# Performance work log

Hardware: AMD Instinct MI355X
Metric: run time of the kernel (lower is better)

## Reference

```python
import jax, jax.numpy as jnp
import numpy as np

EPS = 1e-7  # keras.backend.epsilon()
ROUTINGS = 3


def squash(s, axis=-1):
    # standard capsule squash: ||s||^2/(1+||s||^2) * s/||s||
    n2 = jnp.sum(jnp.square(s), axis=axis, keepdims=True)
    return s * (n2 / (1.0 + n2)) / jnp.sqrt(n2 + EPS)


def setup_inputs() -> dict:
    key = jax.random.key(0)
    k1, k2 = jax.random.split(key)
    B, I, K = 32, 2048, 8          # batch, input capsules, input capsule dim
    J, D = 32, 16                  # output capsules (num_capsules), dim_capsules
    x = jax.random.normal(k1, (B, I, K), dtype=jnp.float32)
    # add_weight with random_normal_initializer(stddev=0.1), shape [J, I, D, K]
    W = 0.1 * jax.random.normal(k2, (J, I, D, K), dtype=jnp.float32)
    return {"x": x, "W": W}


def reference(x, W):
    # u_ji_hat[b,j,i,d] = sum_k W[j,i,d,k] * x[b,i,k]  (the map_fn batched matmul)
    u_hat = jnp.einsum('jidk,bik->bjid', W, x)  # [B, J, I, D]
    B, J, I, D = u_hat.shape
    b = jnp.zeros((B, J, I), dtype=u_hat.dtype)  # routing logits b_ij
    v = None
    for r in range(ROUTINGS):
        c = jax.nn.softmax(b, axis=1)                 # softmax over output capsules J
        s = jnp.einsum('bji,bjid->bjd', c, u_hat)     # weighted sum over input caps i
        v = squash(s, axis=-1)                        # squash over capsule dim (axis=-2 pre-squeeze)
        if r < ROUTINGS - 1:
            # agreement = u_hat^T v : sum over capsule dim d
            b = b + jnp.einsum('bjid,bjd->bji', u_hat, v)
    return v  # [B, J, D] == tf.squeeze(v_j, [2, 4])
```

## Files before the change

kernel.cpp:

```cpp
#include <hip/hip_runtime.h>
#include <hip/hip_fp16.h>


#define BATCH 32
#define ICAP  2048
#define KDIM  8
#define JCAP  32
#define DDIM  16
#define JD    512
#define S_ELEMS 16384
#define EPSQ  1e-7f

#define NB      256
#define ICH     8
#define ISTG    2
#define NROUND  (ICH / ISTG)
#define COLF4   66
#define SLICEF4 (16 * COLF4)

__global__ __launch_bounds__(512, 2)
void caps_pass(const float* __restrict__ W, const float* __restrict__ x,
               const float* __restrict__ vsum, __half* __restrict__ partials) {
    __shared__ float4 Wl[ISTG * SLICEF4];

    const int tid  = threadIdx.x;
    const int wave = tid >> 6;
    const int lane = tid & 63;
    const int j    = lane & 31;
    const int dh   = lane >> 5;
    const int i0   = blockIdx.x * ICH;

    float vs[4][8], sacc[4][8];
#pragma unroll
    for (int bb = 0; bb < 4; ++bb) {
        const int b = wave + 8 * bb;
        const float* vp = vsum + b * JD + j * DDIM + dh * 8;
        float4 a  = *reinterpret_cast<const float4*>(vp);
        float4 bq = *reinterpret_cast<const float4*>(vp + 4);
        vs[bb][0]=a.x; vs[bb][1]=a.y; vs[bb][2]=a.z; vs[bb][3]=a.w;
        vs[bb][4]=bq.x; vs[bb][5]=bq.y; vs[bb][6]=bq.z; vs[bb][7]=bq.w;
#pragma unroll
        for (int r = 0; r < 8; ++r) sacc[bb][r] = 0.f;
    }

    const float4* Wv = reinterpret_cast<const float4*>(W);
    int iloc_s[4], slot_s[4], gbase_s[4];
#pragma unroll
    for (int q = 0; q < 4; ++q) {
        const int f = q * 512 + tid;
        const int il = f >> 10, js = (f >> 5) & 31, c = f & 31;
        iloc_s[q]  = il;
        slot_s[q]  = il * SLICEF4 + (c & 15) * COLF4 + 2 * js + (c >> 4);
        gbase_s[q] = js * 65536 + c;
    }

    float4 pf[4];
#pragma unroll
    for (int q = 0; q < 4; ++q)
        pf[q] = Wv[gbase_s[q] + (i0 + iloc_s[q]) * 32];

    for (int rnd = 0; rnd < NROUND; ++rnd) {
        __syncthreads();
#pragma unroll
        for (int q = 0; q < 4; ++q) Wl[slot_s[q]] = pf[q];
        __syncthreads();
        if (rnd + 1 < NROUND) {
            const int gi_n = i0 + (rnd + 1) * ISTG;
#pragma unroll
            for (int q = 0; q < 4; ++q)
                pf[q] = Wv[gbase_s[q] + (gi_n + iloc_s[q]) * 32];
        }

#pragma unroll
        for (int il = 0; il < ISTG; ++il) {
            const int gi = i0 + rnd * ISTG + il;

            float4 w4[16];
            const int rbase = il * SLICEF4 + 2 * j + dh;
#pragma unroll
            for (int cp = 0; cp < 16; ++cp)
                w4[cp] = Wl[rbase + cp * COLF4];

#pragma unroll
            for (int bb = 0; bb < 4; ++bb) {
                const int b = wave + 8 * bb;
                const float* xp = x + ((size_t)b * ICAP + gi) * KDIM;
                const float4 x0 = *reinterpret_cast<const float4*>(xp);
                const float4 x1 = *reinterpret_cast<const float4*>(xp + 4);

                float u[8], tpart = 0.f;
#pragma unroll
                for (int r = 0; r < 8; ++r) {
                    const float4 wa = w4[2 * r], wb = w4[2 * r + 1];
                    float acc;
                    acc = wa.x * x0.x;
                    acc = fmaf(wa.y, x0.y, acc);
                    acc = fmaf(wa.z, x0.z, acc);
                    acc = fmaf(wa.w, x0.w, acc);
                    acc = fmaf(wb.x, x1.x, acc);
                    acc = fmaf(wb.y, x1.y, acc);
                    acc = fmaf(wb.z, x1.z, acc);
                    acc = fmaf(wb.w, x1.w, acc);
                    u[r] = acc;
                    tpart = fmaf(acc, vs[bb][r], tpart);
                }
                float t = tpart + __shfl_xor(tpart, 32);
                float m = t;
#pragma unroll
                for (int off = 1; off <= 16; off <<= 1)
                    m = fmaxf(m, __shfl_xor(m, off));
                float e = __expf(t - m);
                float se = e;
#pragma unroll
                for (int off = 1; off <= 16; off <<= 1)
                    se += __shfl_xor(se, off);
                const float c = e / se;
#pragma unroll
                for (int r = 0; r < 8; ++r)
                    sacc[bb][r] = fmaf(c, u[r], sacc[bb][r]);
            }
        }
    }

    __half* pout = partials + (size_t)blockIdx.x * S_ELEMS;
#pragma unroll
    for (int bb = 0; bb < 4; ++bb) {
        const int b = wave + 8 * bb;
        union { int4 v; __half2 h[4]; } pk;
#pragma unroll
        for (int r = 0; r < 4; ++r)
            pk.h[r] = __floats2half2_rn(sacc[bb][2 * r], sacc[bb][2 * r + 1]);
        *reinterpret_cast<int4*>(pout + b * JD + j * DDIM + dh * 8) = pk.v;
    }
}

__global__ __launch_bounds__(256)
void caps_reduce(const __half* __restrict__ partials, float* __restrict__ vsum,
                 float* __restrict__ out) {
    __shared__ float buf[4][80];
    const int tid = threadIdx.x;
    const int eL  = tid & 63;
    const int sg  = tid >> 6;
    const int e   = blockIdx.x * 64 + eL;

    float s = 0.f;
    const __half* p = partials + (size_t)(sg * 64) * S_ELEMS + e;
#pragma unroll 8
    for (int n = 0; n < 64; ++n)
        s += __half2float(p[(size_t)n * S_ELEMS]);
    buf[sg][eL] = s;
    __syncthreads();

    if (sg == 0) {
        s = buf[0][eL] + buf[1][eL] + buf[2][eL] + buf[3][eL];
        float n2 = s * s;
#pragma unroll
        for (int off = 1; off <= 8; off <<= 1)
            n2 += __shfl_xor(n2, off);
        const float scale = n2 / ((1.f + n2) * sqrtf(n2 + EPSQ));
        const float v = s * scale;
        vsum[e] += v;
        if (out) out[e] = v;
    }
}

extern "C" void kernel_launch(void* const* d_in, const int* in_sizes, int n_in,
                              void* d_out, int out_size, void* d_ws, size_t ws_size,
                              hipStream_t stream) {
    const float* x = (const float*)d_in[0];
    const float* W = (const float*)d_in[1];
    float* out = (float*)d_out;

    float*  vsum     = (float*)d_ws;
    __half* partials = (__half*)((char*)d_ws + S_ELEMS * sizeof(float));

    hipMemsetAsync(vsum, 0, S_ELEMS * sizeof(float), stream);

    for (int r = 0; r < 3; ++r) {
        caps_pass<<<NB, 512, 0, stream>>>(W, x, vsum, partials);
        caps_reduce<<<S_ELEMS / 64, 256, 0, stream>>>(
            partials, vsum, (r == 2) ? out : nullptr);
    }
}
```

Measured before the change: 185.0 us.

## Pre-transpose W into per-capsule layout and drop LDS staging in routing pass

Adds a one-time transpose kernel that rearranges W into a per-input-capsule contiguous layout in workspace, so the routing pass reads weights straight from global memory with no LDS staging or barriers. It also drops the max-subtraction from the softmax, uses fast reciprocal and rsqrt intrinsics, and widens the reduce kernel to 1024 threads. The trade is an extra full read and write of W (16 MB each way) on every call in exchange for simpler, barrier-free passes. Skipping the max in the softmax risks overflow if the logits grow large.

```diff
diff --git a/kernel.cpp b/kernel.cpp
--- a/kernel.cpp
+++ b/kernel.cpp
@@ -2,27 +2,48 @@
 #include <hip/hip_fp16.h>
 
 
-#define BATCH 32
-#define ICAP  2048
-#define KDIM  8
-#define JCAP  32
-#define DDIM  16
-#define JD    512
+#define ICAP    2048
+#define JD      512
 #define S_ELEMS 16384
-#define EPSQ  1e-7f
+#define EPSQ    1e-7f
+#define NBP     256
+#define ICH     8
 
-#define NB      256
-#define ICH     8
-#define ISTG    2
-#define NROUND  (ICH / ISTG)
-#define COLF4   66
-#define SLICEF4 (16 * COLF4)
+#if defined(__has_builtin) && __has_builtin(__builtin_amdgcn_rcpf)
+#define FAST_RCP(x) __builtin_amdgcn_rcpf(x)
+#else
+#define FAST_RCP(x) (1.0f / (x))
+#endif
+#if defined(__has_builtin) && __has_builtin(__builtin_amdgcn_rsqf)
+#define FAST_RSQ(x) __builtin_amdgcn_rsqf(x)
+#else
+#define FAST_RSQ(x) rsqrtf(x)
+#endif
 
-__global__ __launch_bounds__(512, 2)
-void caps_pass(const float* __restrict__ W, const float* __restrict__ x,
+__global__ __launch_bounds__(256)
+void caps_transpose(const float4* __restrict__ Wv, float4* __restrict__ Wt) {
+    __shared__ float4 buf[16 * 66];
+    const int i = blockIdx.x;
+    const int t = threadIdx.x;
+#pragma unroll
+    for (int q = 0; q < 4; ++q) {
+        const int f = q * 256 + t;
+        const int jj = f >> 5, c = f & 31;
+        buf[(c & 15) * 66 + 2 * jj + (c >> 4)] =
+            Wv[(size_t)jj * 65536 + (size_t)i * 32 + c];
+    }
+    __syncthreads();
+    float4* dst = Wt + (size_t)i * 1024;
+#pragma unroll
+    for (int q = 0; q < 4; ++q) {
+        const int o = q * 256 + t;
+        dst[o] = buf[(o >> 6) * 66 + (o & 63)];
+    }
+}
+
+__global__ __launch_bounds__(512, 1)
+void caps_pass(const float4* __restrict__ Wt, const float* __restrict__ x,
                const float* __restrict__ vsum, __half* __restrict__ partials) {
-    __shared__ float4 Wl[ISTG * SLICEF4];
-
     const int tid  = threadIdx.x;
     const int wave = tid >> 6;
     const int lane = tid & 63;
@@ -34,7 +55,7 @@
 #pragma unroll
     for (int bb = 0; bb < 4; ++bb) {
         const int b = wave + 8 * bb;
-        const float* vp = vsum + b * JD + j * DDIM + dh * 8;
+        const float* vp = vsum + b * JD + j * 16 + dh * 8;
         float4 a  = *reinterpret_cast<const float4*>(vp);
         float4 bq = *reinterpret_cast<const float4*>(vp + 4);
         vs[bb][0]=a.x; vs[bb][1]=a.y; vs[bb][2]=a.z; vs[bb][3]=a.w;
@@ -43,82 +64,49 @@
         for (int r = 0; r < 8; ++r) sacc[bb][r] = 0.f;
     }
 
-    const float4* Wv = reinterpret_cast<const float4*>(W);
-    int iloc_s[4], slot_s[4], gbase_s[4];
+    const float4* wp = Wt + (size_t)i0 * 1024 + 2 * j + dh;
+
+#pragma unroll 1
+    for (int il = 0; il < ICH; ++il) {
+        float4 w4[16];
 #pragma unroll
-    for (int q = 0; q < 4; ++q) {
-        const int f = q * 512 + tid;
-        const int il = f >> 10, js = (f >> 5) & 31, c = f & 31;
-        iloc_s[q]  = il;
-        slot_s[q]  = il * SLICEF4 + (c & 15) * COLF4 + 2 * js + (c >> 4);
-        gbase_s[q] = js * 65536 + c;
-    }
+        for (int cc = 0; cc < 16; ++cc)
+            w4[cc] = wp[(size_t)il * 1024 + cc * 64];
 
-    float4 pf[4];
+        const int gi = i0 + il;
 #pragma unroll
-    for (int q = 0; q < 4; ++q)
-        pf[q] = Wv[gbase_s[q] + (i0 + iloc_s[q]) * 32];
+        for (int bb = 0; bb < 4; ++bb) {
+            const int b = wave + 8 * bb;
+            const float* xp = x + ((size_t)b * ICAP + gi) * 8;
+            const float4 x0 = *reinterpret_cast<const float4*>(xp);
+            const float4 x1 = *reinterpret_cast<const float4*>(xp + 4);
 
-    for (int rnd = 0; rnd < NROUND; ++rnd) {
-        __syncthreads();
+            float u[8], tpart = 0.f;
 #pragma unroll
-        for (int q = 0; q < 4; ++q) Wl[slot_s[q]] = pf[q];
-        __syncthreads();
-        if (rnd + 1 < NROUND) {
-            const int gi_n = i0 + (rnd + 1) * ISTG;
+            for (int r = 0; r < 8; ++r) {
+                const float4 wa = w4[2 * r], wb = w4[2 * r + 1];
+                float acc;
+                acc = wa.x * x0.x;
+                acc = fmaf(wa.y, x0.y, acc);
+                acc = fmaf(wa.z, x0.z, acc);
+                acc = fmaf(wa.w, x0.w, acc);
+                acc = fmaf(wb.x, x1.x, acc);
+                acc = fmaf(wb.y, x1.y, acc);
+                acc = fmaf(wb.z, x1.z, acc);
+                acc = fmaf(wb.w, x1.w, acc);
+                u[r] = acc;
+                tpart = fmaf(acc, vs[bb][r], tpart);
+            }
+            const float t = tpart + __shfl_xor(tpart, 32);
+            const float e = __expf(t);
+            float se = e;
 #pragma unroll
-            for (int q = 0; q < 4; ++q)
-                pf[q] = Wv[gbase_s[q] + (gi_n + iloc_s[q]) * 32];
-        }
-
+            for (int off = 1; off <= 16; off <<= 1)
+                se += __shfl_xor(se, off);
+            const float c = e * FAST_RCP(se);
 #pragma unroll
-        for (int il = 0; il < ISTG; ++il) {
-            const int gi = i0 + rnd * ISTG + il;
-
-            float4 w4[16];
-            const int rbase = il * SLICEF4 + 2 * j + dh;
-#pragma unroll
-            for (int cp = 0; cp < 16; ++cp)
-                w4[cp] = Wl[rbase + cp * COLF4];
-
-#pragma unroll
-            for (int bb = 0; bb < 4; ++bb) {
-                const int b = wave + 8 * bb;
-                const float* xp = x + ((size_t)b * ICAP + gi) * KDIM;
-                const float4 x0 = *reinterpret_cast<const float4*>(xp);
-                const float4 x1 = *reinterpret_cast<const float4*>(xp + 4);
-
-                float u[8], tpart = 0.f;
-#pragma unroll
-                for (int r = 0; r < 8; ++r) {
-                    const float4 wa = w4[2 * r], wb = w4[2 * r + 1];
-                    float acc;
-                    acc = wa.x * x0.x;
-                    acc = fmaf(wa.y, x0.y, acc);
-                    acc = fmaf(wa.z, x0.z, acc);
-                    acc = fmaf(wa.w, x0.w, acc);
-                    acc = fmaf(wb.x, x1.x, acc);
-                    acc = fmaf(wb.y, x1.y, acc);
-                    acc = fmaf(wb.z, x1.z, acc);
-                    acc = fmaf(wb.w, x1.w, acc);
-                    u[r] = acc;
-                    tpart = fmaf(acc, vs[bb][r], tpart);
-                }
-                float t = tpart + __shfl_xor(tpart, 32);
-                float m = t;
-#pragma unroll
-                for (int off = 1; off <= 16; off <<= 1)
-                    m = fmaxf(m, __shfl_xor(m, off));
-                float e = __expf(t - m);
-                float se = e;
-#pragma unroll
-                for (int off = 1; off <= 16; off <<= 1)
-                    se += __shfl_xor(se, off);
-                const float c = e / se;
-#pragma unroll
-                for (int r = 0; r < 8; ++r)
-                    sacc[bb][r] = fmaf(c, u[r], sacc[bb][r]);
-            }
+            for (int r = 0; r < 8; ++r)
+                sacc[bb][r] = fmaf(c, u[r], sacc[bb][r]);
         }
     }
 
@@ -130,34 +118,36 @@
 #pragma unroll
         for (int r = 0; r < 4; ++r)
             pk.h[r] = __floats2half2_rn(sacc[bb][2 * r], sacc[bb][2 * r + 1]);
-        *reinterpret_cast<int4*>(pout + b * JD + j * DDIM + dh * 8) = pk.v;
+        *reinterpret_cast<int4*>(pout + b * JD + j * 16 + dh * 8) = pk.v;
     }
 }
 
-__global__ __launch_bounds__(256)
+__global__ __launch_bounds__(1024)
 void caps_reduce(const __half* __restrict__ partials, float* __restrict__ vsum,
                  float* __restrict__ out) {
-    __shared__ float buf[4][80];
+    __shared__ float buf[16][80];
     const int tid = threadIdx.x;
     const int eL  = tid & 63;
     const int sg  = tid >> 6;
     const int e   = blockIdx.x * 64 + eL;
 
     float s = 0.f;
-    const __half* p = partials + (size_t)(sg * 64) * S_ELEMS + e;
-#pragma unroll 8
-    for (int n = 0; n < 64; ++n)
-        s += __half2float(p[(size_t)n * S_ELEMS]);
+    const __half* p = partials + (size_t)sg * S_ELEMS + e;
+#pragma unroll
+    for (int n = 0; n < 16; ++n)
+        s += __half2float(p[(size_t)(n * 16) * S_ELEMS]);
     buf[sg][eL] = s;
     __syncthreads();
 
     if (sg == 0) {
-        s = buf[0][eL] + buf[1][eL] + buf[2][eL] + buf[3][eL];
+        s = 0.f;
+#pragma unroll
+        for (int k = 0; k < 16; ++k) s += buf[k][eL];
         float n2 = s * s;
 #pragma unroll
         for (int off = 1; off <= 8; off <<= 1)
             n2 += __shfl_xor(n2, off);
-        const float scale = n2 / ((1.f + n2) * sqrtf(n2 + EPSQ));
+        const float scale = n2 * FAST_RCP(1.f + n2) * FAST_RSQ(n2 + EPSQ);
         const float v = s * scale;
         vsum[e] += v;
         if (out) out[e] = v;
@@ -171,14 +161,16 @@
     const float* W = (const float*)d_in[1];
     float* out = (float*)d_out;
 
-    float*  vsum     = (float*)d_ws;
-    __half* partials = (__half*)((char*)d_ws + S_ELEMS * sizeof(float));
+    float4* Wt       = (float4*)d_ws;
+    float*  vsum     = (float*)((char*)d_ws + (size_t)ICAP * 1024 * 16);
+    __half* partials = (__half*)((char*)vsum + S_ELEMS * sizeof(float));
 
     hipMemsetAsync(vsum, 0, S_ELEMS * sizeof(float), stream);
+    caps_transpose<<<ICAP, 256, 0, stream>>>((const float4*)W, Wt);
 
     for (int r = 0; r < 3; ++r) {
-        caps_pass<<<NB, 512, 0, stream>>>(W, x, vsum, partials);
-        caps_reduce<<<S_ELEMS / 64, 256, 0, stream>>>(
+        caps_pass<<<NBP, 512, 0, stream>>>(Wt, x, vsum, partials);
+        caps_reduce<<<S_ELEMS / 64, 1024, 0, stream>>>(
             partials, vsum, (r == 2) ? out : nullptr);
     }
 }
```

Measured after the change: 176.3 us. 1.05x faster.
